# Kernel optimization log

Hardware: AMD Instinct MI355X
Metric: run time of the kernel (lower is better)

## Reference

```python
import jax, jax.numpy as jnp
import numpy as np

EPS = 1e-05
HEAD_DIM = 32


def setup_inputs() -> dict:
    key = jax.random.key(0)
    ks = jax.random.split(key, 8)
    b, c, h, w = 8, 512, 64, 64
    s = 1.0 / np.sqrt(c).astype(np.float32)
    return {
        "q": jax.random.normal(ks[0], (b, c, h, w), jnp.float32),
        "k": jax.random.normal(ks[1], (b, c, h, w), jnp.float32),
        "v": jax.random.normal(ks[2], (b, c, h, w), jnp.float32),
        "Wq": jax.random.normal(ks[3], (c, c), jnp.float32) * s,
        "Wk": jax.random.normal(ks[4], (c, c), jnp.float32) * s,
        "Wv": jax.random.normal(ks[5], (c, c), jnp.float32) * s,
        "Wp": jax.random.normal(ks[6], (c, c), jnp.float32) * s,
        "bp": jax.random.normal(ks[7], (c,), jnp.float32) * 0.02,
    }


def reference(q, k, v, Wq, Wk, Wv, Wp, bp):
    b, c, h, w = q.shape
    n = h * w
    hd = HEAD_DIM
    nh = c // hd

    def proj_heads(x, W):
        # NCHW -> (b, n, c) tokens, then Linear (x @ W.T), then split heads
        t = x.reshape(b, c, n).transpose(0, 2, 1)          # (b, n, c)
        y = jnp.einsum('bnc,dc->bnd', t, W)                # torch Linear: x @ W.T
        return y.reshape(b, n, nh, hd)                     # (b, n, h, d)

    # elu feature map: elu(x) + 1
    Q = jax.nn.elu(proj_heads(q, Wq)) + 1.0
    K = jax.nn.elu(proj_heads(k, Wk)) + 1.0
    V = proj_heads(v, Wv)

    # NOTE: faithful to original einsums — KV contracts over HEADS per token,
    # Z uses K summed over the sequence.
    KV = jnp.einsum('bnhd,bnhm->bnmd', K, V)               # (b, n, d_out=m? -> (b,n,hd,hd))
    Z = 1.0 / (jnp.einsum('bnhd,bhd->bnh', Q, K.sum(axis=1)) + EPS)  # (b, n, h)
    out = jnp.einsum('bnhd,bnmd,bnh->bnhm', Q, KV, Z)      # (b, n, h, m)

    out = out.reshape(b, n, c)                             # merge heads
    out = jnp.einsum('bnc,dc->bnd', out, Wp) + bp          # output projection
    return out.transpose(0, 2, 1).reshape(b, c, h, w)
```

## Files before the change

### kernel.cpp

```cpp
#include <hip/hip_runtime.h>
#include <hip/hip_bf16.h>

#define BATCH 8
#define CD 512
#define NT 4096
#define EPSV 1e-5f

using u16x8 = __attribute__((ext_vector_type(8))) unsigned short;
using u16x4 = __attribute__((ext_vector_type(4))) unsigned short;
using bf8   = __attribute__((ext_vector_type(8))) short;
using f32x4 = __attribute__((ext_vector_type(4))) float;

__device__ __forceinline__ float b2f(unsigned short u) {
    union { unsigned int i; float f; } x; x.i = ((unsigned int)u) << 16; return x.f;
}
__device__ __forceinline__ unsigned short f2b(float f) {
    unsigned int x = __float_as_uint(f);
    unsigned int r = (x + 0x7fffu + ((x >> 16) & 1u)) >> 16;
    return (unsigned short)r;
}
__device__ __forceinline__ unsigned int cvtpk(float a, float b) {
    unsigned int r;
    asm("v_cvt_pk_bf16_f32 %0, %1, %2" : "=v"(r) : "v"(a), "v"(b));
    return r;
}
__device__ __forceinline__ void gload_lds16(const void* g, void* l) {
    __builtin_amdgcn_global_load_lds((const __attribute__((address_space(1))) unsigned int*)g,
                                     (__attribute__((address_space(3))) unsigned int*)l, 16, 0, 0);
}
__device__ __forceinline__ int swz8(int r) { return (r ^ (r >> 3)) & 7; }

__global__ __launch_bounds__(256)
void wconv(const float* __restrict__ W0, const float* __restrict__ W1,
           const float* __restrict__ W2, const float* __restrict__ W3,
           unsigned short* __restrict__ Wb) {
    const float* src = (blockIdx.y == 0) ? W0 : (blockIdx.y == 1) ? W1 : (blockIdx.y == 2) ? W2 : W3;
    unsigned short* dst = Wb + (size_t)blockIdx.y * CD * CD;
    const int base = blockIdx.x * 4096 + threadIdx.x * 16;
    u16x8 o0, o1;
    #pragma unroll
    for (int i = 0; i < 4; ++i) {
        float4 v = *reinterpret_cast<const float4*>(src + base + i * 4);
        unsigned short* t = (i < 2) ? (unsigned short*)&o0 : (unsigned short*)&o1;
        t[(i & 1) * 4 + 0] = f2b(v.x); t[(i & 1) * 4 + 1] = f2b(v.y);
        t[(i & 1) * 4 + 2] = f2b(v.z); t[(i & 1) * 4 + 3] = f2b(v.w);
    }
    *(u16x8*)(dst + base)     = o0;
    *(u16x8*)(dst + base + 8) = o1;
}

__global__ __launch_bounds__(512, 4)
void proj_gemm_all(const float* __restrict__ q, const float* __restrict__ k,
                   const float* __restrict__ v, const unsigned short* __restrict__ Wb,
                   unsigned short* __restrict__ Qp, unsigned short* __restrict__ Kp,
                   unsigned short* __restrict__ Vp, float* __restrict__ Kpart) {
    __shared__ __align__(16) unsigned short Xs[32 * 512];
    __shared__ __align__(16) unsigned short Wsb[2][256 * 32];
    const int nper = gridDim.x >> 3;
    const int work = (blockIdx.x & 7) * nper + (blockIdx.x >> 3);
    const int mat  = work / 1024;
    const int rem  = work - mat * 1024;
    const int b    = rem >> 7;
    const int tile = rem & 127;
    const int n0   = tile * 32;
    const float* Xb = (mat == 0 ? q : mat == 1 ? k : v) + (size_t)b * CD * NT;
    const unsigned short* W = Wb + (size_t)mat * CD * CD;
    unsigned short* Tb = (mat == 0 ? Qp : mat == 1 ? Kp : Vp) + (size_t)b * NT * CD;
    const int act = (mat < 2);

    const int tid = threadIdx.x, lane = tid & 63, wv = tid >> 6;
    const int r16 = lane & 15, g = lane >> 4;

    #pragma unroll
    for (int i = 0; i < 2; ++i) {
        const int s  = i * 512 + tid;
        const int c0 = (s >> 3) * 4;
        const int t0 = (s & 7) * 4;
        const float* p = Xb + (size_t)c0 * NT + n0 + t0;
        float4 r0 = *(const float4*)(p);
        float4 r1 = *(const float4*)(p + NT);
        float4 r2 = *(const float4*)(p + 2 * NT);
        float4 r3 = *(const float4*)(p + 3 * NT);
        float a0[4] = {r0.x, r0.y, r0.z, r0.w};
        float a1[4] = {r1.x, r1.y, r1.z, r1.w};
        float a2[4] = {r2.x, r2.y, r2.z, r2.w};
        float a3[4] = {r3.x, r3.y, r3.z, r3.w};
        #pragma unroll
        for (int j = 0; j < 4; ++j) {
            uint2 u;
            u.x = cvtpk(a0[j], a1[j]);
            u.y = cvtpk(a2[j], a3[j]);
            const int row  = t0 + j;
            const int byte = (row * 1024 + c0 * 2) ^ (swz8(row) << 4);
            *(uint2*)((char*)Xs + byte) = u;
        }
    }
    __syncthreads();

    const int rl0 = lane >> 2;
    const int sl  = lane & 3;
    #define ISSUEW(D0I, KC, BUF) do {                                              \
        _Pragma("unroll") for (int it_ = 0; it_ < 2; ++it_) {                      \
            const int rl_ = it_ * 16 + rl0;                                        \
            const int q_  = sl ^ ((rl_ >> 1) & 3);                                 \
            gload_lds16(W + (size_t)((D0I) * 256 + wv * 32 + rl_) * CD + (KC) * 32 + q_ * 8, \
                        (char*)Wsb + (BUF) * 16384 + wv * 2048 + it_ * 1024 + lane * 16); \
        }                                                                          \
    } while (0)

    #define READAF(AF, KC) do {                                                    \
        _Pragma("unroll") for (int m_ = 0; m_ < 2; ++m_) {                         \
            const int r_ = m_ * 16 + r16;                                          \
            AF[m_] = *(const bf8*)((const char*)Xs +                               \
                     ((r_ * 1024 + (KC) * 64 + g * 16) ^ (swz8(r_) << 4)));        \
        }                                                                          \
    } while (0)

    #define READBF(BUF) do {                                                       \
        const char* Wcur_ = (const char*)Wsb + (BUF) * 16384 + wv * 2048;          \
        _Pragma("unroll") for (int j_ = 0; j_ < 2; ++j_) {                         \
            const int lr_ = j_ * 16 + r16;                                         \
            bfr[j_] = *(const bf8*)(Wcur_ + lr_ * 64 + ((g ^ ((lr_ >> 1) & 3)) * 16)); \
        }                                                                          \
    } while (0)

    #define DOMFMA(AF) do {                                                        \
        __builtin_amdgcn_s_setprio(1);                                             \
        _Pragma("unroll") for (int m_ = 0; m_ < 2; ++m_)                           \
        _Pragma("unroll") for (int j_ = 0; j_ < 2; ++j_)                           \
            acc[m_][j_] = __builtin_amdgcn_mfma_f32_16x16x32_bf16(AF[m_], bfr[j_], acc[m_][j_], 0, 0, 0); \
        __builtin_amdgcn_s_setprio(0);                                             \
    } while (0)

    for (int d0i = 0; d0i < 2; ++d0i) {
        f32x4 acc[2][2];
        #pragma unroll
        for (int m = 0; m < 2; ++m)
            #pragma unroll
            for (int j = 0; j < 2; ++j)
                acc[m][j] = (f32x4){0.f, 0.f, 0.f, 0.f};

        bf8 afA[2], afB[2], bfr[2];
        ISSUEW(d0i, 0, 0);
        READAF(afA, 0);

        #pragma unroll
        for (int kp2 = 0; kp2 < 8; ++kp2) {
            const int kc = kp2 * 2;
            ISSUEW(d0i, kc + 1, 1);
            asm volatile("s_waitcnt vmcnt(2)" ::: "memory");
            __builtin_amdgcn_sched_barrier(0);
            READBF(0);
            READAF(afB, kc + 1);
            DOMFMA(afA);
            if (kp2 < 7) {
                ISSUEW(d0i, kc + 2, 0);
                asm volatile("s_waitcnt vmcnt(2)" ::: "memory");
            } else {
                asm volatile("s_waitcnt vmcnt(0)" ::: "memory");
            }
            __builtin_amdgcn_sched_barrier(0);
            READBF(1);
            if (kp2 < 7) READAF(afA, kc + 2);
            DOMFMA(afB);
        }

        float kacc[2] = {0.f, 0.f};
        #pragma unroll
        for (int m = 0; m < 2; ++m) {
            const int ib = n0 + m * 16 + (g << 2);
            #pragma unroll
            for (int j = 0; j < 2; ++j) {
                const int jb = d0i * 256 + wv * 32 + j * 16 + r16;
                f32x4 vv = acc[m][j];
                #pragma unroll
                for (int r = 0; r < 4; ++r) {
                    float val = vv[r];
                    if (act) val = (val > 0.f) ? (val + 1.f) : __expf(val);
                    if (mat == 1) kacc[j] += val;
                    Tb[(size_t)(ib + r) * CD + jb] = f2b(val);
                }
            }
        }
        if (mat == 1) {
            #pragma unroll
            for (int j = 0; j < 2; ++j) {
                float s = kacc[j];
                s += __shfl_xor(s, 16, 64);
                s += __shfl_xor(s, 32, 64);
                if (lane < 16) {
                    const int jb = d0i * 256 + wv * 32 + j * 16 + lane;
                    Kpart[(size_t)(b * 128 + tile) * CD + jb] = s;
                }
            }
        }
    }
    #undef ISSUEW
    #undef READAF
    #undef READBF
    #undef DOMFMA
}

__global__ __launch_bounds__(512)
void ksum_red2(const float* __restrict__ Kpart, float* __restrict__ Ks) {
    const int b = blockIdx.x, c = threadIdx.x;
    float s = 0.f;
    #pragma unroll 8
    for (int t = 0; t < 128; ++t) s += Kpart[(size_t)(b * 128 + t) * CD + c];
    Ks[b * CD + c] = s;
}

__global__ __launch_bounds__(256)
void gemm_final(const unsigned short* __restrict__ Wp, const unsigned short* __restrict__ Tm,
                float* __restrict__ out, const float* __restrict__ bias) {
    __shared__ __align__(16) unsigned short Asm[128 * 64];
    __shared__ __align__(16) unsigned short Bsm[128 * 64];
    const int nper = gridDim.x >> 3;
    const int work = (blockIdx.x & 7) * nper + (blockIdx.x >> 3);
    const int i0 = (work & 3) * 128;
    const int j0 = ((work >> 2) & 31) * 128;
    const int b  = work >> 7;
    const unsigned short* Bb = Tm + (size_t)b * NT * CD;
    const int tid  = threadIdx.x;
    const int lane = tid & 63;
    const int wv   = tid >> 6;
    const int wi = wv >> 1, wj = wv & 1;

    f32x4 acc[4][4];
    #pragma unroll
    for (int m = 0; m < 4; ++m)
        #pragma unroll
        for (int j = 0; j < 4; ++j)
            acc[m][j] = (f32x4){0.f, 0.f, 0.f, 0.f};

    for (int k0 = 0; k0 < CD; k0 += 64) {
        #pragma unroll
        for (int it = 0; it < 4; ++it) {
            const int idx = it * 256 + tid;
            const int r = idx >> 3, p = idx & 7;
            const int ps = p ^ (r & 7);
            gload_lds16(Wp + (size_t)(i0 + r) * CD + k0 + ps * 8, (char*)Asm + idx * 16);
            gload_lds16(Bb + (size_t)(j0 + r) * CD + k0 + ps * 8, (char*)Bsm + idx * 16);
        }
        __syncthreads();
        #pragma unroll
        for (int kk = 0; kk < 2; ++kk) {
            bf8 af[4], bfr[4];
            #pragma unroll
            for (int m = 0; m < 4; ++m) {
                const int r  = wi * 64 + m * 16 + (lane & 15);
                const int kp = kk * 4 + (lane >> 4);
                af[m] = *(const bf8*)((const char*)Asm + r * 128 + ((kp ^ (r & 7)) * 16));
            }
            #pragma unroll
            for (int j = 0; j < 4; ++j) {
                const int r  = wj * 64 + j * 16 + (lane & 15);
                const int kp = kk * 4 + (lane >> 4);
                bfr[j] = *(const bf8*)((const char*)Bsm + r * 128 + ((kp ^ (r & 7)) * 16));
            }
            #pragma unroll
            for (int m = 0; m < 4; ++m)
                #pragma unroll
                for (int j = 0; j < 4; ++j)
                    acc[m][j] = __builtin_amdgcn_mfma_f32_16x16x32_bf16(af[m], bfr[j], acc[m][j], 0, 0, 0);
        }
        __syncthreads();
    }

    #pragma unroll
    for (int m = 0; m < 4; ++m) {
        const int ib = i0 + wi * 64 + m * 16 + (lane >> 4) * 4;
        #pragma unroll
        for (int j = 0; j < 4; ++j) {
            const int jb = j0 + wj * 64 + j * 16 + (lane & 15);
            f32x4 v = acc[m][j];
            #pragma unroll
            for (int r = 0; r < 4; ++r)
                out[(size_t)b * CD * NT + (size_t)(ib + r) * NT + jb] = v[r] + bias[ib + r];
        }
    }
}

__global__ __launch_bounds__(256)
void middle2(const unsigned short* __restrict__ Q, const unsigned short* __restrict__ K,
             const unsigned short* __restrict__ V, const float* __restrict__ Ksum,
             unsigned short* __restrict__ T) {
    __shared__ __align__(16) unsigned short sV[4][512];
    __shared__ __align__(16) unsigned short sP[4][16][32];
    const int b = blockIdx.y;
    const int tid = threadIdx.x;
    const int w = tid >> 6, lane = tid & 63;
    const int r16 = lane & 15, g = lane >> 4;
    const int n0 = blockIdx.x * 16 + w * 4;
    const unsigned short* Qb = Q + ((size_t)b * NT + n0) * CD;
    const unsigned short* Kb = K + ((size_t)b * NT + n0) * CD;
    const unsigned short* Vb = V + ((size_t)b * NT + n0) * CD;
    unsigned short* Tb = T + ((size_t)b * NT + n0) * CD;
    const int fragoff = r16 * 32 + g * 8;

    {
        const int r = lane >> 2, cq = lane & 3;
        *(u16x4*)&sP[w][r][16 + cq * 4] = (u16x4){0, 0, 0, 0};
    }

    const float* ksp = Ksum + b * CD + fragoff;
    float ks[8];
    {
        float4 a0 = *(const float4*)ksp;
        float4 a1 = *(const float4*)(ksp + 4);
        ks[0] = a0.x; ks[1] = a0.y; ks[2] = a0.z; ks[3] = a0.w;
        ks[4] = a1.x; ks[5] = a1.y; ks[6] = a1.z; ks[7] = a1.w;
    }
    unsigned short* sVw = &sV[w][0];

    for (int t = 0; t < 4; ++t) {
        asm volatile("s_waitcnt lgkmcnt(0)" ::: "memory");
        __builtin_amdgcn_sched_barrier(0);
        gload_lds16(Vb + (size_t)t * CD + lane * 8, (char*)sVw + lane * 16);

        const bf8 qf = *(const bf8*)(Qb + (size_t)t * CD + fragoff);
        const bf8 kf = *(const bf8*)(Kb + (size_t)t * CD + fragoff);

        f32x4 s = {0.f, 0.f, 0.f, 0.f};
        s = __builtin_amdgcn_mfma_f32_16x16x32_bf16(kf, qf, s, 0, 0, 0);

        float part = 0.f;
        #pragma unroll
        for (int e = 0; e < 8; ++e) part += b2f((unsigned short)qf[e]) * ks[e];
        part += __shfl_xor(part, 16, 64);
        part += __shfl_xor(part, 32, 64);
        const float z = 1.f / (part + EPSV);

        u16x4 pw;
        #pragma unroll
        for (int r = 0; r < 4; ++r) pw[r] = f2b(s[r] * z);
        *(u16x4*)&sP[w][r16][g * 4] = pw;

        asm volatile("s_waitcnt vmcnt(0) lgkmcnt(0)" ::: "memory");
        __builtin_amdgcn_sched_barrier(0);

        const bf8 pb = *(const bf8*)&sP[w][r16][g * 8];
        bf8 va0 = {}, va1 = {};
        if (g < 2) {
            #pragma unroll
            for (int e = 0; e < 8; ++e) {
                va0[e] = (short)sVw[(g * 8 + e) * 32 + r16];
                va1[e] = (short)sVw[(g * 8 + e) * 32 + 16 + r16];
            }
        }

        f32x4 o0 = {0.f, 0.f, 0.f, 0.f}, o1 = {0.f, 0.f, 0.f, 0.f};
        o0 = __builtin_amdgcn_mfma_f32_16x16x32_bf16(va0, pb, o0, 0, 0, 0);
        o1 = __builtin_amdgcn_mfma_f32_16x16x32_bf16(va1, pb, o1, 0, 0, 0);

        u16x4 w0, w1;
        #pragma unroll
        for (int r = 0; r < 4; ++r) { w0[r] = f2b(o0[r]); w1[r] = f2b(o1[r]); }
        *(u16x4*)(Tb + (size_t)t * CD + r16 * 32 + g * 4)      = w0;
        *(u16x4*)(Tb + (size_t)t * CD + r16 * 32 + 16 + g * 4) = w1;
    }
}

extern "C" void kernel_launch(void* const* d_in, const int* in_sizes, int n_in,
                              void* d_out, int out_size, void* d_ws, size_t ws_size,
                              hipStream_t stream) {
    const float* q  = (const float*)d_in[0];
    const float* k  = (const float*)d_in[1];
    const float* v  = (const float*)d_in[2];
    const float* Wq = (const float*)d_in[3];
    const float* Wk = (const float*)d_in[4];
    const float* Wv = (const float*)d_in[5];
    const float* Wp = (const float*)d_in[6];
    const float* bp = (const float*)d_in[7];
    float* out = (float*)d_out;

    const size_t slab = (size_t)BATCH * NT * CD;
    unsigned short* Qp = (unsigned short*)d_ws;
    unsigned short* Kp = Qp + slab;
    unsigned short* Vp = Kp + slab;
    unsigned short* Tm = Vp + slab;
    unsigned short* Wb = Tm + slab;
    float* Kpart = (float*)(Wb + 4 * (size_t)CD * CD);
    float* Ks    = Kpart + (size_t)BATCH * 128 * CD;

    wconv<<<dim3(64, 4), 256, 0, stream>>>(Wq, Wk, Wv, Wp, Wb);

    const unsigned short* Wpb = Wb + (size_t)3 * CD * CD;

    proj_gemm_all<<<3072, 512, 0, stream>>>(q, k, v, Wb, Qp, Kp, Vp, Kpart);

    ksum_red2<<<8, 512, 0, stream>>>(Kpart, Ks);

    middle2<<<dim3(256, 8), 256, 0, stream>>>(Qp, Kp, Vp, Ks, Tm);

    gemm_final<<<1024, 256, 0, stream>>>(Wpb, Tm, out, bp);
}
```

Baseline: 190.1 us.

## Triple-buffer weight loads and merge both output halves into one pipelined loop

The projection GEMM's weight streaming moves from a double buffer to a triple buffer, with loads issued three chunks ahead. The two separate d0i passes become one continuous 32-chunk pipeline, so the prefetch no longer drains and restarts at the half boundary. Both accumulator sets are kept live and written in a single epilogue. In exchange, LDS use rises by 16 KB per block and more registers stay live at once, which may reduce occupancy under the (512,4) launch bounds.

```diff
diff --git a/kernel.cpp b/kernel.cpp
--- a/kernel.cpp
+++ b/kernel.cpp
@@ -55,7 +55,7 @@
                    unsigned short* __restrict__ Qp, unsigned short* __restrict__ Kp,
                    unsigned short* __restrict__ Vp, float* __restrict__ Kpart) {
     __shared__ __align__(16) unsigned short Xs[32 * 512];
-    __shared__ __align__(16) unsigned short Wsb[2][256 * 32];
+    __shared__ __align__(16) unsigned short Wsb[3][256 * 32];
     const int nper = gridDim.x >> 3;
     const int work = (blockIdx.x & 7) * nper + (blockIdx.x >> 3);
     const int mat  = work / 1024;
@@ -99,19 +99,19 @@
 
     const int rl0 = lane >> 2;
     const int sl  = lane & 3;
-    #define ISSUEW(D0I, KC, BUF) do {                                              \
+    #define ISSUEW(CC) do {                                                        \
         _Pragma("unroll") for (int it_ = 0; it_ < 2; ++it_) {                      \
             const int rl_ = it_ * 16 + rl0;                                        \
             const int q_  = sl ^ ((rl_ >> 1) & 3);                                 \
-            gload_lds16(W + (size_t)((D0I) * 256 + wv * 32 + rl_) * CD + (KC) * 32 + q_ * 8, \
-                        (char*)Wsb + (BUF) * 16384 + wv * 2048 + it_ * 1024 + lane * 16); \
+            gload_lds16(W + (size_t)(((CC) >> 4) * 256 + wv * 32 + rl_) * CD + ((CC) & 15) * 32 + q_ * 8, \
+                        (char*)Wsb + ((CC) % 3) * 16384 + wv * 2048 + it_ * 1024 + lane * 16); \
         }                                                                          \
     } while (0)
 
-    #define READAF(AF, KC) do {                                                    \
+    #define READAF(KC) do {                                                        \
         _Pragma("unroll") for (int m_ = 0; m_ < 2; ++m_) {                         \
             const int r_ = m_ * 16 + r16;                                          \
-            AF[m_] = *(const bf8*)((const char*)Xs +                               \
+            af[m_] = *(const bf8*)((const char*)Xs +                               \
                      ((r_ * 1024 + (KC) * 64 + g * 16) ^ (swz8(r_) << 4)));        \
         }                                                                          \
     } while (0)
@@ -124,74 +124,75 @@
         }                                                                          \
     } while (0)
 
-    #define DOMFMA(AF) do {                                                        \
+    #define DOMFMA(ACC) do {                                                       \
         __builtin_amdgcn_s_setprio(1);                                             \
         _Pragma("unroll") for (int m_ = 0; m_ < 2; ++m_)                           \
         _Pragma("unroll") for (int j_ = 0; j_ < 2; ++j_)                           \
-            acc[m_][j_] = __builtin_amdgcn_mfma_f32_16x16x32_bf16(AF[m_], bfr[j_], acc[m_][j_], 0, 0, 0); \
+            ACC[m_][j_] = __builtin_amdgcn_mfma_f32_16x16x32_bf16(af[m_], bfr[j_], ACC[m_][j_], 0, 0, 0); \
         __builtin_amdgcn_s_setprio(0);                                             \
     } while (0)
 
-    for (int d0i = 0; d0i < 2; ++d0i) {
-        f32x4 acc[2][2];
-        #pragma unroll
-        for (int m = 0; m < 2; ++m)
-            #pragma unroll
-            for (int j = 0; j < 2; ++j)
-                acc[m][j] = (f32x4){0.f, 0.f, 0.f, 0.f};
-
-        bf8 afA[2], afB[2], bfr[2];
-        ISSUEW(d0i, 0, 0);
-        READAF(afA, 0);
-
-        #pragma unroll
-        for (int kp2 = 0; kp2 < 8; ++kp2) {
-            const int kc = kp2 * 2;
-            ISSUEW(d0i, kc + 1, 1);
-            asm volatile("s_waitcnt vmcnt(2)" ::: "memory");
-            __builtin_amdgcn_sched_barrier(0);
-            READBF(0);
-            READAF(afB, kc + 1);
-            DOMFMA(afA);
-            if (kp2 < 7) {
-                ISSUEW(d0i, kc + 2, 0);
-                asm volatile("s_waitcnt vmcnt(2)" ::: "memory");
-            } else {
-                asm volatile("s_waitcnt vmcnt(0)" ::: "memory");
-            }
-            __builtin_amdgcn_sched_barrier(0);
-            READBF(1);
-            if (kp2 < 7) READAF(afA, kc + 2);
-            DOMFMA(afB);
-        }
-
-        float kacc[2] = {0.f, 0.f};
-        #pragma unroll
-        for (int m = 0; m < 2; ++m) {
-            const int ib = n0 + m * 16 + (g << 2);
-            #pragma unroll
-            for (int j = 0; j < 2; ++j) {
-                const int jb = d0i * 256 + wv * 32 + j * 16 + r16;
-                f32x4 vv = acc[m][j];
-                #pragma unroll
-                for (int r = 0; r < 4; ++r) {
-                    float val = vv[r];
-                    if (act) val = (val > 0.f) ? (val + 1.f) : __expf(val);
-                    if (mat == 1) kacc[j] += val;
-                    Tb[(size_t)(ib + r) * CD + jb] = f2b(val);
+    #define CHUNK(CC, ACC) do {                                                    \
+        if ((CC) <= 29)      asm volatile("s_waitcnt vmcnt(4)" ::: "memory");      \
+        else if ((CC) == 30) asm volatile("s_waitcnt vmcnt(2)" ::: "memory");      \
+        else                 asm volatile("s_waitcnt vmcnt(0)" ::: "memory");      \
+        __builtin_amdgcn_sched_barrier(0);                                         \
+        READBF((CC) % 3);                                                          \
+        READAF((CC) & 15);                                                         \
+        asm volatile("s_waitcnt lgkmcnt(0)" ::: "memory");                         \
+        __builtin_amdgcn_sched_barrier(0);                                         \
+        if ((CC) + 3 < 32) ISSUEW((CC) + 3);                                       \
+        DOMFMA(ACC);                                                               \
+    } while (0)
+
+    f32x4 accA[2][2], accB[2][2];
+    #pragma unroll
+    for (int m = 0; m < 2; ++m)
+        #pragma unroll
+        for (int j = 0; j < 2; ++j) {
+            accA[m][j] = (f32x4){0.f, 0.f, 0.f, 0.f};
+            accB[m][j] = (f32x4){0.f, 0.f, 0.f, 0.f};
+        }
+
+    bf8 af[2], bfr[2];
+    ISSUEW(0); ISSUEW(1); ISSUEW(2);
+    #pragma unroll
+    for (int cc = 0; cc < 16; ++cc) CHUNK(cc, accA);
+    #pragma unroll
+    for (int cc = 16; cc < 32; ++cc) CHUNK(cc, accB);
+
+    float kaccA[2] = {0.f, 0.f}, kaccB[2] = {0.f, 0.f};
+    #pragma unroll
+    for (int m = 0; m < 2; ++m) {
+        const int ib = n0 + m * 16 + (g << 2);
+        #pragma unroll
+        for (int j = 0; j < 2; ++j) {
+            const int jbA = wv * 32 + j * 16 + r16;
+            const int jbB = 256 + jbA;
+            f32x4 vA = accA[m][j], vB = accB[m][j];
+            #pragma unroll
+            for (int r = 0; r < 4; ++r) {
+                float a = vA[r], c = vB[r];
+                if (act) {
+                    a = (a > 0.f) ? (a + 1.f) : __expf(a);
+                    c = (c > 0.f) ? (c + 1.f) : __expf(c);
                 }
-            }
-        }
-        if (mat == 1) {
-            #pragma unroll
-            for (int j = 0; j < 2; ++j) {
-                float s = kacc[j];
-                s += __shfl_xor(s, 16, 64);
-                s += __shfl_xor(s, 32, 64);
-                if (lane < 16) {
-                    const int jb = d0i * 256 + wv * 32 + j * 16 + lane;
-                    Kpart[(size_t)(b * 128 + tile) * CD + jb] = s;
-                }
+                if (mat == 1) { kaccA[j] += a; kaccB[j] += c; }
+                Tb[(size_t)(ib + r) * CD + jbA] = f2b(a);
+                Tb[(size_t)(ib + r) * CD + jbB] = f2b(c);
+            }
+        }
+    }
+    if (mat == 1) {
+        #pragma unroll
+        for (int j = 0; j < 2; ++j) {
+            float sA = kaccA[j], sB = kaccB[j];
+            sA += __shfl_xor(sA, 16, 64); sA += __shfl_xor(sA, 32, 64);
+            sB += __shfl_xor(sB, 16, 64); sB += __shfl_xor(sB, 32, 64);
+            if (lane < 16) {
+                float* kp = Kpart + (size_t)(b * 128 + tile) * CD;
+                kp[wv * 32 + j * 16 + lane]       = sA;
+                kp[256 + wv * 32 + j * 16 + lane] = sB;
             }
         }
     }
@@ -199,6 +200,7 @@
     #undef READAF
     #undef READBF
     #undef DOMFMA
+    #undef CHUNK
 }
 
 __global__ __launch_bounds__(512)
```

Result: slower. 196.8 us (+3.5%).
